# Performance work log

Hardware: AMD Instinct MI355X
Metric: run time of the kernel (lower is better)

The kernel has to match this reference:

```python
import jax, jax.numpy as jnp
from jax import lax
import numpy as np

L = 8            # NMF rank (n_components)
NMF_ITERS = 50   # fixed multiplicative-update iterations
EPS = 1.1920929e-07  # float32 machine eps, as sklearn uses


def nmf_mu(V, key):
    """Multiplicative-update NMF (Frobenius loss), sklearn-style random init.
    V: [T, M] nonnegative. Returns W:[T,L], H:[L,M]."""
    T, M = V.shape
    kW, kH = jax.random.split(key)
    avg = jnp.sqrt(jnp.mean(V) / L)
    W0 = avg * jax.random.uniform(kW, (T, L), dtype=V.dtype)
    H0 = avg * jax.random.uniform(kH, (L, M), dtype=V.dtype)

    def step(carry, _):
        W, H = carry
        # H update: H *= (W^T V) / (W^T W H)
        H = H * (W.T @ V) / (W.T @ W @ H + EPS)
        # W update: W *= (V H^T) / (W H H^T)
        W = W * (V @ H.T) / (W @ (H @ H.T) + EPS)
        return (W, H), None

    (W, H), _ = lax.scan(step, (W0, H0), None, length=NMF_ITERS)
    return W, H


def pointwise_conv(w, x):
    # 1x1x1 Conv3d == channel mix: w [C_out, C_in], x [n, C_in, D, H, W]
    return jnp.einsum('oc,ncdhw->nodhw', w, x)


def setup_inputs() -> dict:
    key = jax.random.key(0)
    k0, k1, k2, k3, k4 = jax.random.split(key, 5)
    C = 64
    eps = jax.random.normal(k0, (1, C, 16, 64, 64), dtype=jnp.float32)
    s = 1.0 / np.sqrt(C)  # keep pre-activation variance ~1 (like torch init scale)
    w_pre = jax.random.normal(k1, (C, C), dtype=jnp.float32) * s
    b_pre = jax.random.normal(k2, (C,), dtype=jnp.float32) * s
    w_post1 = jax.random.normal(k3, (C, C), dtype=jnp.float32) * s
    w_post2 = jax.random.normal(k4, (C, C), dtype=jnp.float32) * s
    return {"eps": eps, "w_pre": w_pre, "b_pre": b_pre,
            "w_post1": w_post1, "w_post2": w_post2}


def reference(eps, w_pre, b_pre, w_post1, w_post2):
    n, t, k, a, b = eps.shape
    # xi_pre: 1x1x1 conv + bias + ReLU (ReLU guarantees nonnegative NMF input)
    Vst = jax.nn.relu(pointwise_conv(w_pre, eps) + b_pre[None, :, None, None, None])
    V = Vst.reshape(t, k * a * b)  # n == 1
    W, H = nmf_mu(V, jax.random.key(0))
    Vst_hat = (W @ H).reshape(n, t, k, a, b)
    error = jnp.linalg.norm(Vst - Vst_hat)  # torch.dist (Frobenius)
    # xi_post: conv(no bias) -> ReLU -> conv(no bias)
    y = jax.nn.relu(pointwise_conv(w_post1, Vst_hat))
    eps_hat = pointwise_conv(w_post2, y)
    return eps_hat, error
```

## Files before the change

kernel.cpp:

```cpp
#include <hip/hip_runtime.h>
#include <stdint.h>

#define JAX_PARTITIONABLE 1

constexpr int kC = 64;
constexpr int kS = 65536;
constexpr int kL = 8;
constexpr int kIters = 50;
constexpr int kBlocks = 256;
constexpr int kThreads = 512;
constexpr int kCols = 256;
constexpr int kGroups = 4;
constexpr int kEntries = 576;
constexpr int kHP = 260;
constexpr int kVP = 68;
constexpr int kNP = 258;
constexpr float kEps = 1.1920929e-07f;

#define AGENT __HIP_MEMORY_SCOPE_AGENT

struct Ctl {
  unsigned root;  unsigned pad0[31];
  unsigned leaf[16][32];
  float mean_sum; float err_sum; float pad1[30];
  float B[3][kGroups][kEntries];
};

__device__ __forceinline__ uint2 tf2x32(unsigned k0, unsigned k1,
                                        unsigned x0, unsigned x1) {
  unsigned k2 = k0 ^ k1 ^ 0x1BD11BDAu;
  x0 += k0; x1 += k1;
#define TF_RND(r) { x0 += x1; x1 = (x1 << (r)) | (x1 >> (32 - (r))); x1 ^= x0; }
  TF_RND(13) TF_RND(15) TF_RND(26) TF_RND(6)
  x0 += k1; x1 += k2 + 1u;
  TF_RND(17) TF_RND(29) TF_RND(16) TF_RND(24)
  x0 += k2; x1 += k0 + 2u;
  TF_RND(13) TF_RND(15) TF_RND(26) TF_RND(6)
  x0 += k0; x1 += k1 + 3u;
  TF_RND(17) TF_RND(29) TF_RND(16) TF_RND(24)
  x0 += k1; x1 += k2 + 4u;
  TF_RND(13) TF_RND(15) TF_RND(26) TF_RND(6)
  x0 += k2; x1 += k0 + 5u;
#undef TF_RND
  return make_uint2(x0, x1);
}

__device__ __forceinline__ float u01(unsigned b) {
  return __uint_as_float((b >> 9) | 0x3f800000u) - 1.0f;
}

__device__ __forceinline__ void gridbar(Ctl* ctl, unsigned& round) {
  ++round;
  __syncthreads();
  if (threadIdx.x == 0) {
    const unsigned leaf = blockIdx.x & 15u;
    unsigned a = __hip_atomic_fetch_add(&ctl->leaf[leaf][0], 1u,
                                        __ATOMIC_RELAXED, AGENT);
    if (a == round * 16u - 1u)
      __hip_atomic_fetch_add(&ctl->root, 1u, __ATOMIC_RELAXED, AGENT);
    const unsigned target = round * 16u;
    while (__hip_atomic_load(&ctl->root, __ATOMIC_RELAXED, AGENT) < target)
      __builtin_amdgcn_s_sleep(1);
    __builtin_amdgcn_fence(__ATOMIC_ACQUIRE, "agent");
  }
  __syncthreads();
}

__global__ void init_ctl(unsigned* ws) {
  const unsigned n = (unsigned)(sizeof(Ctl) / 4);
  for (unsigned i = blockIdx.x * blockDim.x + threadIdx.x; i < n;
       i += gridDim.x * blockDim.x)
    ws[i] = 0u;
}

__global__ __launch_bounds__(kThreads, 2) void fsam_nmf(
    const float* __restrict__ eps, const float* __restrict__ w_pre,
    const float* __restrict__ b_pre, const float* __restrict__ w_post1,
    const float* __restrict__ w_post2, float* __restrict__ out, Ctl* ctl) {
  __shared__ __align__(16) float Vt[kCols][kVP];
  __shared__ __align__(16) float Hs[kL][kHP];
  __shared__ __align__(16) float Pn[4][kL][kNP];
  __shared__ __align__(16) float Pv[8][512];
  __shared__ __align__(16) float Ph[16][64];
  __shared__ __align__(16) float Pw[8][64];
  __shared__ __align__(16) float Ws[kC][kL];
  __shared__ __align__(16) float WtWs[64];
  __shared__ __align__(16) float hhts[64];
  __shared__ float reds[8];

  const int tid = threadIdx.x;
  const int g = tid >> 7;
  const int p = tid & 127;
  const int obase = g * 16;
  const int sb = blockIdx.x * kCols;
  unsigned bar_round = 0;

  float vreg[2][16];
#pragma unroll
  for (int o = 0; o < 16; ++o) { vreg[0][o] = b_pre[obase + o]; vreg[1][o] = vreg[0][o]; }
  for (int c = 0; c < kC; ++c) {
    const float2 e2 = *(const float2*)(eps + (size_t)c * kS + sb + 2 * p);
#pragma unroll
    for (int o = 0; o < 16; ++o) {
      const float w = w_pre[(obase + o) * kC + c];
      vreg[0][o] = fmaf(w, e2.x, vreg[0][o]);
      vreg[1][o] = fmaf(w, e2.y, vreg[1][o]);
    }
  }
  float lsum = 0.0f;
#pragma unroll
  for (int col = 0; col < 2; ++col) {
#pragma unroll
    for (int o = 0; o < 16; ++o) {
      vreg[col][o] = fmaxf(vreg[col][o], 0.0f);
      lsum += vreg[col][o];
    }
#pragma unroll
    for (int k = 0; k < 4; ++k)
      *(float4*)&Vt[2 * p + col][obase + 4 * k] =
          make_float4(vreg[col][4 * k], vreg[col][4 * k + 1],
                      vreg[col][4 * k + 2], vreg[col][4 * k + 3]);
  }
  {
    float r = lsum;
#pragma unroll
    for (int off = 32; off > 0; off >>= 1) r += __shfl_down(r, off, 64);
    if ((tid & 63) == 0) reds[tid >> 6] = r;
    __syncthreads();
    if (tid == 0) {
      float sm = 0.0f;
#pragma unroll
      for (int w = 0; w < 8; ++w) sm += reds[w];
      __hip_atomic_fetch_add(&ctl->mean_sum, sm, __ATOMIC_RELAXED, AGENT);
    }
  }
  gridbar(ctl, bar_round);
  const float avg = sqrtf(
      __hip_atomic_load(&ctl->mean_sum, __ATOMIC_RELAXED, AGENT) *
      (1.0f / (4194304.0f * 8.0f)));

#if JAX_PARTITIONABLE
  const uint2 kw = tf2x32(0u, 0u, 0u, 0u);
  const uint2 kh = tf2x32(0u, 0u, 0u, 1u);
#else
  const uint2 A0 = tf2x32(0u, 0u, 0u, 2u);
  const uint2 A1 = tf2x32(0u, 0u, 1u, 3u);
  const uint2 kw = make_uint2(A0.x, A1.x);
  const uint2 kh = make_uint2(A0.y, A1.y);
#endif
  if (tid < 256) {
    const int s = sb + tid;
#if JAX_PARTITIONABLE
#pragma unroll
    for (int l = 0; l < kL; ++l) {
      uint2 r = tf2x32(kh.x, kh.y, 0u, (unsigned)(l * kS + s));
      Hs[l][tid] = avg * u01(r.x ^ r.y);
    }
#else
#pragma unroll
    for (int l = 0; l < 4; ++l) {
      unsigned i = (unsigned)(l * kS + s);
      uint2 r = tf2x32(kh.x, kh.y, i, i + 262144u);
      Hs[l][tid] = avg * u01(r.x);
      Hs[l + 4][tid] = avg * u01(r.y);
    }
#endif
  }
  {
#if JAX_PARTITIONABLE
    uint2 r0 = tf2x32(kw.x, kw.y, 0u, (unsigned)tid);
    (&Ws[0][0])[tid] = avg * u01(r0.x ^ r0.y);
#else
    if (tid < 256) {
      uint2 r = tf2x32(kw.x, kw.y, (unsigned)tid, (unsigned)(tid + 256));
      (&Ws[0][0])[tid] = avg * u01(r.x);
      (&Ws[0][0])[tid + 256] = avg * u01(r.y);
    }
#endif
  }
  __syncthreads();

  for (int it = 0; it < kIters; ++it) {
    {
      const int e = tid & 63, chunk = tid >> 6, cb = chunk * 8;
      const int l = e >> 3, j = e & 7;
      float s = 0.0f;
#pragma unroll
      for (int cc = 0; cc < 8; ++cc)
        s = fmaf(Ws[cb + cc][l], Ws[cb + cc][j], s);
      Pw[chunk][e] = s;
    }
    {
      float num[2][kL] = {};
#pragma unroll
      for (int ci = 0; ci < 16; ++ci) {
        const int c = obase + ci;
        const float4 w0 = *(const float4*)&Ws[c][0];
        const float4 w1 = *(const float4*)&Ws[c][4];
        const float v0 = vreg[0][ci], v1 = vreg[1][ci];
        num[0][0] = fmaf(v0, w0.x, num[0][0]); num[0][1] = fmaf(v0, w0.y, num[0][1]);
        num[0][2] = fmaf(v0, w0.z, num[0][2]); num[0][3] = fmaf(v0, w0.w, num[0][3]);
        num[0][4] = fmaf(v0, w1.x, num[0][4]); num[0][5] = fmaf(v0, w1.y, num[0][5]);
        num[0][6] = fmaf(v0, w1.z, num[0][6]); num[0][7] = fmaf(v0, w1.w, num[0][7]);
        num[1][0] = fmaf(v1, w0.x, num[1][0]); num[1][1] = fmaf(v1, w0.y, num[1][1]);
        num[1][2] = fmaf(v1, w0.z, num[1][2]); num[1][3] = fmaf(v1, w0.w, num[1][3]);
        num[1][4] = fmaf(v1, w1.x, num[1][4]); num[1][5] = fmaf(v1, w1.y, num[1][5]);
        num[1][6] = fmaf(v1, w1.z, num[1][6]); num[1][7] = fmaf(v1, w1.w, num[1][7]);
      }
#pragma unroll
      for (int l = 0; l < kL; ++l)
        *(float2*)&Pn[g][l][2 * p] = make_float2(num[0][l], num[1][l]);
    }
    __syncthreads();
    const int col = tid & 255, lh = tid >> 8;
    float h[kL], nm[4];
#pragma unroll
    for (int l = 0; l < kL; ++l) h[l] = Hs[l][col];
#pragma unroll
    for (int k = 0; k < 4; ++k) {
      const int l = lh * 4 + k;
      nm[k] = Pn[0][l][col] + Pn[1][l][col] + Pn[2][l][col] + Pn[3][l][col];
    }
    if (tid < 64) {
      float s = 0.0f;
#pragma unroll
      for (int r = 0; r < 8; ++r) s += Pw[r][tid];
      WtWs[tid] = s;
    }
    __syncthreads();
#pragma unroll
    for (int k = 0; k < 4; ++k) {
      const int l = lh * 4 + k;
      const float4 a = *(const float4*)&WtWs[l * kL];
      const float4 b = *(const float4*)&WtWs[l * kL + 4];
      float d = kEps;
      d = fmaf(a.x, h[0], d); d = fmaf(a.y, h[1], d);
      d = fmaf(a.z, h[2], d); d = fmaf(a.w, h[3], d);
      d = fmaf(b.x, h[4], d); d = fmaf(b.y, h[5], d);
      d = fmaf(b.z, h[6], d); d = fmaf(b.w, h[7], d);
      Hs[l][col] = h[l] * nm[k] / d;
    }
    __syncthreads();
    if (tid < 256) {
      const int tle = tid & 15, rng = tid >> 4;
      const int j0 = (tle >> 2) * 2, l0 = (tle & 3) * 2;
      const int s0 = rng * 16;
      float a00 = 0, a01 = 0, a10 = 0, a11 = 0;
      for (int s4 = s0; s4 < s0 + 16; s4 += 4) {
        const float4 x0 = *(const float4*)&Hs[j0][s4];
        const float4 x1 = *(const float4*)&Hs[j0 + 1][s4];
        const float4 y0 = *(const float4*)&Hs[l0][s4];
        const float4 y1 = *(const float4*)&Hs[l0 + 1][s4];
        a00 = fmaf(x0.x, y0.x, a00); a00 = fmaf(x0.y, y0.y, a00);
        a00 = fmaf(x0.z, y0.z, a00); a00 = fmaf(x0.w, y0.w, a00);
        a01 = fmaf(x0.x, y1.x, a01); a01 = fmaf(x0.y, y1.y, a01);
        a01 = fmaf(x0.z, y1.z, a01); a01 = fmaf(x0.w, y1.w, a01);
        a10 = fmaf(x1.x, y0.x, a10); a10 = fmaf(x1.y, y0.y, a10);
        a10 = fmaf(x1.z, y0.z, a10); a10 = fmaf(x1.w, y0.w, a10);
        a11 = fmaf(x1.x, y1.x, a11); a11 = fmaf(x1.y, y1.y, a11);
        a11 = fmaf(x1.z, y1.z, a11); a11 = fmaf(x1.w, y1.w, a11);
      }
      const int sw = (rng & 1) | ((rng & 2) << 2);
      Ph[rng][(j0 * 8 + l0) ^ sw] = a00;
      Ph[rng][(j0 * 8 + l0 + 1) ^ sw] = a01;
      Ph[rng][((j0 + 1) * 8 + l0) ^ sw] = a10;
      Ph[rng][((j0 + 1) * 8 + l0 + 1) ^ sw] = a11;
    }
    {
      const int tile = tid & 63, rng = tid >> 6;
      const int cq = tile & 15, lp = tile >> 4;
      const int cb = cq * 4, lb = lp * 2;
      float acc[4][2] = {};
      for (int s4 = rng * 32; s4 < rng * 32 + 32; s4 += 4) {
        const float4 h0 = *(const float4*)&Hs[lb][s4];
        const float4 h1 = *(const float4*)&Hs[lb + 1][s4];
        const float4 va = *(const float4*)&Vt[s4][cb];
        const float4 vb = *(const float4*)&Vt[s4 + 1][cb];
        const float4 vc = *(const float4*)&Vt[s4 + 2][cb];
        const float4 vd = *(const float4*)&Vt[s4 + 3][cb];
        acc[0][0] = fmaf(va.x, h0.x, acc[0][0]); acc[0][1] = fmaf(va.x, h1.x, acc[0][1]);
        acc[1][0] = fmaf(va.y, h0.x, acc[1][0]); acc[1][1] = fmaf(va.y, h1.x, acc[1][1]);
        acc[2][0] = fmaf(va.z, h0.x, acc[2][0]); acc[2][1] = fmaf(va.z, h1.x, acc[2][1]);
        acc[3][0] = fmaf(va.w, h0.x, acc[3][0]); acc[3][1] = fmaf(va.w, h1.x, acc[3][1]);
        acc[0][0] = fmaf(vb.x, h0.y, acc[0][0]); acc[0][1] = fmaf(vb.x, h1.y, acc[0][1]);
        acc[1][0] = fmaf(vb.y, h0.y, acc[1][0]); acc[1][1] = fmaf(vb.y, h1.y, acc[1][1]);
        acc[2][0] = fmaf(vb.z, h0.y, acc[2][0]); acc[2][1] = fmaf(vb.z, h1.y, acc[2][1]);
        acc[3][0] = fmaf(vb.w, h0.y, acc[3][0]); acc[3][1] = fmaf(vb.w, h1.y, acc[3][1]);
        acc[0][0] = fmaf(vc.x, h0.z, acc[0][0]); acc[0][1] = fmaf(vc.x, h1.z, acc[0][1]);
        acc[1][0] = fmaf(vc.y, h0.z, acc[1][0]); acc[1][1] = fmaf(vc.y, h1.z, acc[1][1]);
        acc[2][0] = fmaf(vc.z, h0.z, acc[2][0]); acc[2][1] = fmaf(vc.z, h1.z, acc[2][1]);
        acc[3][0] = fmaf(vc.w, h0.z, acc[3][0]); acc[3][1] = fmaf(vc.w, h1.z, acc[3][1]);
        acc[0][0] = fmaf(vd.x, h0.w, acc[0][0]); acc[0][1] = fmaf(vd.x, h1.w, acc[0][1]);
        acc[1][0] = fmaf(vd.y, h0.w, acc[1][0]); acc[1][1] = fmaf(vd.y, h1.w, acc[1][1]);
        acc[2][0] = fmaf(vd.z, h0.w, acc[2][0]); acc[2][1] = fmaf(vd.z, h1.w, acc[2][1]);
        acc[3][0] = fmaf(vd.w, h0.w, acc[3][0]); acc[3][1] = fmaf(vd.w, h1.w, acc[3][1]);
      }
#pragma unroll
      for (int j = 0; j < 4; ++j) {
        const int sl = lp * 128 + j * 32 + ((cq ^ (j << 2) ^ lp) << 1);
        *(float2*)&Pv[rng][sl] = make_float2(acc[j][0], acc[j][1]);
      }
    }
    __syncthreads();
    float* Bg = &ctl->B[it % 3][blockIdx.x & 3][0];
    {
      const int c = tid >> 3, l = tid & 7;
      const int cq = c >> 2, j = c & 3, lp = l >> 1;
      const int slot = lp * 128 + j * 32 + ((cq ^ (j << 2) ^ lp) << 1) + (l & 1);
      float v = 0.0f;
#pragma unroll
      for (int r = 0; r < 8; ++r) v += Pv[r][slot];
      __hip_atomic_fetch_add(&Bg[tid], v, __ATOMIC_RELAXED, AGENT);
    }
    if (tid < 64) {
      float v = 0.0f;
#pragma unroll
      for (int r = 0; r < 16; ++r)
        v += Ph[r][tid ^ ((r & 1) | ((r & 2) << 2))];
      __hip_atomic_fetch_add(&Bg[512 + tid], v, __ATOMIC_RELAXED, AGENT);
    }
    if ((blockIdx.x >> 2) == 4) {
      float* nb = &ctl->B[(it + 1) % 3][blockIdx.x & 3][0];
      __hip_atomic_store(&nb[tid], 0.0f, __ATOMIC_RELAXED, AGENT);
      if (tid < 64)
        __hip_atomic_store(&nb[512 + tid], 0.0f, __ATOMIC_RELAXED, AGENT);
    }

    gridbar(ctl, bar_round);

    const float* Bb = &ctl->B[it % 3][0][0];
    float v = Bb[tid] + Bb[kEntries + tid] + Bb[2 * kEntries + tid] +
              Bb[3 * kEntries + tid];
    if (tid < 64) {
      hhts[tid] = Bb[512 + tid] + Bb[kEntries + 512 + tid] +
                  Bb[2 * kEntries + 512 + tid] + Bb[3 * kEntries + 512 + tid];
    }
    __syncthreads();
    float wn;
    {
      const int c0 = tid >> 3, l0 = tid & 7;
      const float4 w0 = *(const float4*)&Ws[c0][0];
      const float4 w1 = *(const float4*)&Ws[c0][4];
      float d = kEps;
      d = fmaf(w0.x, hhts[l0], d);      d = fmaf(w0.y, hhts[8 + l0], d);
      d = fmaf(w0.z, hhts[16 + l0], d); d = fmaf(w0.w, hhts[24 + l0], d);
      d = fmaf(w1.x, hhts[32 + l0], d); d = fmaf(w1.y, hhts[40 + l0], d);
      d = fmaf(w1.z, hhts[48 + l0], d); d = fmaf(w1.w, hhts[56 + l0], d);
      wn = (&Ws[0][0])[tid] * v / d;
    }
    __syncthreads();
    (&Ws[0][0])[tid] = wn;
    __syncthreads();
  }

  float h2[2][kL];
#pragma unroll
  for (int l = 0; l < kL; ++l) {
    const float2 t2 = *(const float2*)&Hs[l][2 * p];
    h2[0][l] = t2.x; h2[1][l] = t2.y;
  }
  float errp = 0.0f;
  float vh[2][16];
#pragma unroll
  for (int ci = 0; ci < 16; ++ci) {
    const int c = obase + ci;
    const float4 w0 = *(const float4*)&Ws[c][0];
    const float4 w1 = *(const float4*)&Ws[c][4];
#pragma unroll
    for (int colx = 0; colx < 2; ++colx) {
      float t = 0.0f;
      t = fmaf(w0.x, h2[colx][0], t); t = fmaf(w0.y, h2[colx][1], t);
      t = fmaf(w0.z, h2[colx][2], t); t = fmaf(w0.w, h2[colx][3], t);
      t = fmaf(w1.x, h2[colx][4], t); t = fmaf(w1.y, h2[colx][5], t);
      t = fmaf(w1.z, h2[colx][6], t); t = fmaf(w1.w, h2[colx][7], t);
      vh[colx][ci] = t;
      const float d = vreg[colx][ci] - t;
      errp = fmaf(d, d, errp);
    }
  }
#pragma unroll
  for (int colx = 0; colx < 2; ++colx)
#pragma unroll
    for (int k = 0; k < 4; ++k)
      *(float4*)&Vt[2 * p + colx][obase + 4 * k] =
          make_float4(vh[colx][4 * k], vh[colx][4 * k + 1],
                      vh[colx][4 * k + 2], vh[colx][4 * k + 3]);
  {
    float r = errp;
#pragma unroll
    for (int off = 32; off > 0; off >>= 1) r += __shfl_down(r, off, 64);
    __syncthreads();
    if ((tid & 63) == 0) reds[tid >> 6] = r;
    __syncthreads();
    if (tid == 0) {
      float sm = 0.0f;
#pragma unroll
      for (int w = 0; w < 8; ++w) sm += reds[w];
      __hip_atomic_fetch_add(&ctl->err_sum, sm, __ATOMIC_RELAXED, AGENT);
    }
  }
  __syncthreads();
  float ya[2][16] = {};
  for (int cb = 0; cb < 16; ++cb) {
    const float4 v0 = *(const float4*)&Vt[2 * p][cb * 4];
    const float4 v1 = *(const float4*)&Vt[2 * p + 1][cb * 4];
#pragma unroll
    for (int o = 0; o < 16; ++o) {
      const float* wr = &w_post1[(obase + o) * kC + cb * 4];
      ya[0][o] = fmaf(wr[0], v0.x, ya[0][o]); ya[1][o] = fmaf(wr[0], v1.x, ya[1][o]);
      ya[0][o] = fmaf(wr[1], v0.y, ya[0][o]); ya[1][o] = fmaf(wr[1], v1.y, ya[1][o]);
      ya[0][o] = fmaf(wr[2], v0.z, ya[0][o]); ya[1][o] = fmaf(wr[2], v1.z, ya[1][o]);
      ya[0][o] = fmaf(wr[3], v0.w, ya[0][o]); ya[1][o] = fmaf(wr[3], v1.w, ya[1][o]);
    }
  }
  __syncthreads();
#pragma unroll
  for (int colx = 0; colx < 2; ++colx)
#pragma unroll
    for (int k = 0; k < 4; ++k)
      *(float4*)&Vt[2 * p + colx][obase + 4 * k] =
          make_float4(fmaxf(ya[colx][4 * k], 0.0f), fmaxf(ya[colx][4 * k + 1], 0.0f),
                      fmaxf(ya[colx][4 * k + 2], 0.0f), fmaxf(ya[colx][4 * k + 3], 0.0f));
  __syncthreads();
  float oa[2][16] = {};
  for (int cb = 0; cb < 16; ++cb) {
    const float4 v0 = *(const float4*)&Vt[2 * p][cb * 4];
    const float4 v1 = *(const float4*)&Vt[2 * p + 1][cb * 4];
#pragma unroll
    for (int o = 0; o < 16; ++o) {
      const float* wr = &w_post2[(obase + o) * kC + cb * 4];
      oa[0][o] = fmaf(wr[0], v0.x, oa[0][o]); oa[1][o] = fmaf(wr[0], v1.x, oa[1][o]);
      oa[0][o] = fmaf(wr[1], v0.y, oa[0][o]); oa[1][o] = fmaf(wr[1], v1.y, oa[1][o]);
      oa[0][o] = fmaf(wr[2], v0.z, oa[0][o]); oa[1][o] = fmaf(wr[2], v1.z, oa[1][o]);
      oa[0][o] = fmaf(wr[3], v0.w, oa[0][o]); oa[1][o] = fmaf(wr[3], v1.w, oa[1][o]);
    }
  }
#pragma unroll
  for (int o = 0; o < 16; ++o)
    *(float2*)&out[(size_t)(obase + o) * kS + sb + 2 * p] =
        make_float2(oa[0][o], oa[1][o]);

  gridbar(ctl, bar_round);
  if (blockIdx.x == 0 && tid == 0)
    out[(size_t)kC * kS] =
        sqrtf(__hip_atomic_load(&ctl->err_sum, __ATOMIC_RELAXED, AGENT));
}

extern "C" void kernel_launch(void* const* d_in, const int* in_sizes, int n_in,
                              void* d_out, int out_size, void* d_ws, size_t ws_size,
                              hipStream_t stream) {
  (void)in_sizes; (void)n_in; (void)out_size; (void)ws_size;
  const float* eps     = (const float*)d_in[0];
  const float* w_pre   = (const float*)d_in[1];
  const float* b_pre   = (const float*)d_in[2];
  const float* w_post1 = (const float*)d_in[3];
  const float* w_post2 = (const float*)d_in[4];
  float* out = (float*)d_out;
  Ctl* ctl = (Ctl*)d_ws;

  init_ctl<<<64, 256, 0, stream>>>((unsigned*)d_ws);
  fsam_nmf<<<kBlocks, kThreads, 0, stream>>>(eps, w_pre, b_pre, w_post1,
                                             w_post2, out, ctl);
}
```

Before: 626.6 us.

## Double-buffer W, fold WtW into spare threads, and halve atomic reduction groups

W is double-buffered in shared memory, which removes one barrier in the W update. W^T W is now computed by the last 64 threads in a single 64-long loop, overlapped with the numerator partial sums, rather than as 8-chunk partials followed by a separate reduce step. The H update now has adjacent threads splitting one column, and one more barrier goes away. The cross-block atomic accumulation uses 2 groups instead of 4, so fewer global reads happen after the grid barrier, at the cost of more atomic contention per address.

Measured after the change: 699.5 us. 11.6% more time.

```diff
diff --git a/kernel.cpp b/kernel.cpp
--- a/kernel.cpp
+++ b/kernel.cpp
@@ -10,7 +10,7 @@
 constexpr int kBlocks = 256;
 constexpr int kThreads = 512;
 constexpr int kCols = 256;
-constexpr int kGroups = 4;
+constexpr int kGroups = 2;
 constexpr int kEntries = 576;
 constexpr int kHP = 260;
 constexpr int kVP = 68;
@@ -82,8 +82,7 @@
   __shared__ __align__(16) float Pn[4][kL][kNP];
   __shared__ __align__(16) float Pv[8][512];
   __shared__ __align__(16) float Ph[16][64];
-  __shared__ __align__(16) float Pw[8][64];
-  __shared__ __align__(16) float Ws[kC][kL];
+  __shared__ __align__(16) float Ws[2][kC][kL];
   __shared__ __align__(16) float WtWs[64];
   __shared__ __align__(16) float hhts[64];
   __shared__ float reds[8];
@@ -169,34 +168,26 @@
   {
 #if JAX_PARTITIONABLE
     uint2 r0 = tf2x32(kw.x, kw.y, 0u, (unsigned)tid);
-    (&Ws[0][0])[tid] = avg * u01(r0.x ^ r0.y);
+    (&Ws[0][0][0])[tid] = avg * u01(r0.x ^ r0.y);
 #else
     if (tid < 256) {
       uint2 r = tf2x32(kw.x, kw.y, (unsigned)tid, (unsigned)(tid + 256));
-      (&Ws[0][0])[tid] = avg * u01(r.x);
-      (&Ws[0][0])[tid + 256] = avg * u01(r.y);
+      (&Ws[0][0][0])[tid] = avg * u01(r.x);
+      (&Ws[0][0][0])[tid + 256] = avg * u01(r.y);
     }
 #endif
   }
   __syncthreads();
 
   for (int it = 0; it < kIters; ++it) {
-    {
-      const int e = tid & 63, chunk = tid >> 6, cb = chunk * 8;
-      const int l = e >> 3, j = e & 7;
-      float s = 0.0f;
-#pragma unroll
-      for (int cc = 0; cc < 8; ++cc)
-        s = fmaf(Ws[cb + cc][l], Ws[cb + cc][j], s);
-      Pw[chunk][e] = s;
-    }
+    const int cur = it & 1, nxt = cur ^ 1;
     {
       float num[2][kL] = {};
 #pragma unroll
       for (int ci = 0; ci < 16; ++ci) {
         const int c = obase + ci;
-        const float4 w0 = *(const float4*)&Ws[c][0];
-        const float4 w1 = *(const float4*)&Ws[c][4];
+        const float4 w0 = *(const float4*)&Ws[cur][c][0];
+        const float4 w1 = *(const float4*)&Ws[cur][c][4];
         const float v0 = vreg[0][ci], v1 = vreg[1][ci];
         num[0][0] = fmaf(v0, w0.x, num[0][0]); num[0][1] = fmaf(v0, w0.y, num[0][1]);
         num[0][2] = fmaf(v0, w0.z, num[0][2]); num[0][3] = fmaf(v0, w0.w, num[0][3]);
@@ -211,34 +202,36 @@
       for (int l = 0; l < kL; ++l)
         *(float2*)&Pn[g][l][2 * p] = make_float2(num[0][l], num[1][l]);
     }
-    __syncthreads();
-    const int col = tid & 255, lh = tid >> 8;
-    float h[kL], nm[4];
-#pragma unroll
-    for (int l = 0; l < kL; ++l) h[l] = Hs[l][col];
-#pragma unroll
-    for (int k = 0; k < 4; ++k) {
-      const int l = lh * 4 + k;
-      nm[k] = Pn[0][l][col] + Pn[1][l][col] + Pn[2][l][col] + Pn[3][l][col];
-    }
-    if (tid < 64) {
+    if (tid >= 448) {
+      const int e = tid - 448, l = e >> 3, j = e & 7;
       float s = 0.0f;
-#pragma unroll
-      for (int r = 0; r < 8; ++r) s += Pw[r][tid];
-      WtWs[tid] = s;
-    }
-    __syncthreads();
-#pragma unroll
-    for (int k = 0; k < 4; ++k) {
-      const int l = lh * 4 + k;
-      const float4 a = *(const float4*)&WtWs[l * kL];
-      const float4 b = *(const float4*)&WtWs[l * kL + 4];
-      float d = kEps;
-      d = fmaf(a.x, h[0], d); d = fmaf(a.y, h[1], d);
-      d = fmaf(a.z, h[2], d); d = fmaf(a.w, h[3], d);
-      d = fmaf(b.x, h[4], d); d = fmaf(b.y, h[5], d);
-      d = fmaf(b.z, h[6], d); d = fmaf(b.w, h[7], d);
-      Hs[l][col] = h[l] * nm[k] / d;
+      for (int c = 0; c < kC; ++c)
+        s = fmaf(Ws[cur][c][l], Ws[cur][c][j], s);
+      WtWs[e] = s;
+    }
+    __syncthreads();
+    {
+      const int col = tid >> 1, lh = tid & 1;
+      float h[kL], nm[4];
+#pragma unroll
+      for (int l = 0; l < kL; ++l) h[l] = Hs[l][col];
+#pragma unroll
+      for (int k = 0; k < 4; ++k) {
+        const int l = lh * 4 + k;
+        nm[k] = Pn[0][l][col] + Pn[1][l][col] + Pn[2][l][col] + Pn[3][l][col];
+      }
+#pragma unroll
+      for (int k = 0; k < 4; ++k) {
+        const int l = lh * 4 + k;
+        const float4 a = *(const float4*)&WtWs[l * kL];
+        const float4 b = *(const float4*)&WtWs[l * kL + 4];
+        float d = kEps;
+        d = fmaf(a.x, h[0], d); d = fmaf(a.y, h[1], d);
+        d = fmaf(a.z, h[2], d); d = fmaf(a.w, h[3], d);
+        d = fmaf(b.x, h[4], d); d = fmaf(b.y, h[5], d);
+        d = fmaf(b.z, h[6], d); d = fmaf(b.w, h[7], d);
+        Hs[l][col] = h[l] * nm[k] / d;
+      }
     }
     __syncthreads();
     if (tid < 256) {
@@ -302,7 +295,7 @@
       }
     }
     __syncthreads();
-    float* Bg = &ctl->B[it % 3][blockIdx.x & 3][0];
+    float* Bg = &ctl->B[it % 3][blockIdx.x & 1][0];
     {
       const int c = tid >> 3, l = tid & 7;
       const int cq = c >> 2, j = c & 3, lp = l >> 1;
@@ -319,8 +312,8 @@
         v += Ph[r][tid ^ ((r & 1) | ((r & 2) << 2))];
       __hip_atomic_fetch_add(&Bg[512 + tid], v, __ATOMIC_RELAXED, AGENT);
     }
-    if ((blockIdx.x >> 2) == 4) {
-      float* nb = &ctl->B[(it + 1) % 3][blockIdx.x & 3][0];
+    if ((blockIdx.x >> 1) == 8) {
+      float* nb = &ctl->B[(it + 1) % 3][blockIdx.x & 1][0];
       __hip_atomic_store(&nb[tid], 0.0f, __ATOMIC_RELAXED, AGENT);
       if (tid < 64)
         __hip_atomic_store(&nb[512 + tid], 0.0f, __ATOMIC_RELAXED, AGENT);
@@ -329,30 +322,25 @@
     gridbar(ctl, bar_round);
 
     const float* Bb = &ctl->B[it % 3][0][0];
-    float v = Bb[tid] + Bb[kEntries + tid] + Bb[2 * kEntries + tid] +
-              Bb[3 * kEntries + tid];
-    if (tid < 64) {
-      hhts[tid] = Bb[512 + tid] + Bb[kEntries + 512 + tid] +
-                  Bb[2 * kEntries + 512 + tid] + Bb[3 * kEntries + 512 + tid];
-    }
-    __syncthreads();
-    float wn;
+    const float v = Bb[tid] + Bb[kEntries + tid];
+    if (tid < 64)
+      hhts[tid] = Bb[512 + tid] + Bb[kEntries + 512 + tid];
+    __syncthreads();
     {
       const int c0 = tid >> 3, l0 = tid & 7;
-      const float4 w0 = *(const float4*)&Ws[c0][0];
-      const float4 w1 = *(const float4*)&Ws[c0][4];
+      const float4 w0 = *(const float4*)&Ws[cur][c0][0];
+      const float4 w1 = *(const float4*)&Ws[cur][c0][4];
       float d = kEps;
       d = fmaf(w0.x, hhts[l0], d);      d = fmaf(w0.y, hhts[8 + l0], d);
       d = fmaf(w0.z, hhts[16 + l0], d); d = fmaf(w0.w, hhts[24 + l0], d);
       d = fmaf(w1.x, hhts[32 + l0], d); d = fmaf(w1.y, hhts[40 + l0], d);
       d = fmaf(w1.z, hhts[48 + l0], d); d = fmaf(w1.w, hhts[56 + l0], d);
-      wn = (&Ws[0][0])[tid] * v / d;
-    }
-    __syncthreads();
-    (&Ws[0][0])[tid] = wn;
-    __syncthreads();
-  }
-
+      (&Ws[nxt][0][0])[tid] = (&Ws[cur][0][0])[tid] * v / d;
+    }
+    __syncthreads();
+  }
+
+  const int fin = kIters & 1;
   float h2[2][kL];
 #pragma unroll
   for (int l = 0; l < kL; ++l) {
@@ -364,8 +352,8 @@
 #pragma unroll
   for (int ci = 0; ci < 16; ++ci) {
     const int c = obase + ci;
-    const float4 w0 = *(const float4*)&Ws[c][0];
-    const float4 w1 = *(const float4*)&Ws[c][4];
+    const float4 w0 = *(const float4*)&Ws[fin][c][0];
+    const float4 w1 = *(const float4*)&Ws[fin][c][4];
 #pragma unroll
     for (int colx = 0; colx < 2; ++colx) {
       float t = 0.0f;
```
